# Performance work log

Measured on AMD Instinct MI355X. Metric: run time of the kernel, lower is better.

Reference implementation:

```python
import jax, jax.numpy as jnp
import numpy as np

B, K, D, V = 4096, 128, 512, 128000


def setup_inputs() -> dict:
    key = jax.random.key(0)
    k1, k2, k3 = jax.random.split(key, 3)
    inp = jax.random.normal(k1, (B, D), dtype=jnp.float32)
    indices = jax.random.randint(k2, (B, K), 0, V, dtype=jnp.int64)
    # xavier_uniform: bound = sqrt(6/(fan_in+fan_out)) for weight [V, D]
    bound = float(np.sqrt(6.0 / (V + D)))
    weight = jax.random.uniform(k3, (V, D), dtype=jnp.float32, minval=-bound, maxval=bound)
    bias = jnp.zeros((V,), dtype=jnp.float32)
    return {"inp": inp, "indices": indices, "sparse": 1, "weight": weight, "bias": bias}


def reference(inp, indices, sparse, weight, bias):
    if sparse:
        # gather per-sample weight rows [B, K, D] and bias [B, K], then batched dot
        w = weight[indices]          # [B, K, D]
        b = bias[indices]            # [B, K]
        out = jnp.einsum('bkd,bd->bk', w, inp) + b
        return out
    else:
        return inp @ weight.T + bias
```

## Files before the change

### kernel.cpp

```cpp
#include <hip/hip_runtime.h>
#include <stdint.h>


constexpr int Kc = 128;
constexpr int Dc = 512;
constexpr int Vc = 128000;

typedef float f4 __attribute__((ext_vector_type(4)));

__global__ __launch_bounds__(256) void SparseProjection_kernel(
    const float* __restrict__ inp,
    const int*   __restrict__ indices,
    const float* __restrict__ weight,
    const float* __restrict__ bias,
    float*       __restrict__ out)
{
    const int b    = blockIdx.x;
    const int tid  = threadIdx.x;
    const int lane = tid & 63;
    const int wave = tid >> 6;

    const float4* inp_row = (const float4*)(inp + (size_t)b * Dc);
    const float4 a0 = inp_row[lane];
    const float4 a1 = inp_row[64 + lane];

    const int* idx_base  = indices + (size_t)b * Kc;
    float*     out_base  = out     + (size_t)b * Kc;

    #pragma unroll 4
    for (int i = 0; i < 32; ++i) {
        const int k   = wave * 32 + i;
        const int idx = idx_base[k];
        const float4* wrow = (const float4*)(weight + (size_t)idx * Dc);

        const float4 w0 = wrow[lane];
        const float4 w1 = wrow[64 + lane];

        float s = a0.x * w0.x + a0.y * w0.y + a0.z * w0.z + a0.w * w0.w
                + a1.x * w1.x + a1.y * w1.y + a1.z * w1.z + a1.w * w1.w;

        #pragma unroll
        for (int off = 32; off > 0; off >>= 1)
            s += __shfl_xor(s, off, 64);

        if (lane == 0)
            out_base[k] = s + bias[idx];
    }
}


__global__ __launch_bounds__(256) void hist_kernel(
    const int* __restrict__ idx, unsigned int* __restrict__ counts, int n)
{
    int i      = blockIdx.x * blockDim.x + threadIdx.x;
    int stride = gridDim.x * blockDim.x;
    for (; i < n; i += stride)
        atomicAdd(&counts[idx[i]], 1u);
}

__global__ __launch_bounds__(256) void scan1_kernel(
    const unsigned int* __restrict__ counts, unsigned int* __restrict__ partials)
{
    __shared__ unsigned int sm[256];
    const int c = blockIdx.x;
    const int t = threadIdx.x;
    unsigned int a = counts[c * 512 + 2 * t] + counts[c * 512 + 2 * t + 1];
    sm[t] = a;
    __syncthreads();
    for (int off = 128; off > 0; off >>= 1) {
        if (t < off) sm[t] += sm[t + off];
        __syncthreads();
    }
    if (t == 0) partials[c] = sm[0];
}

__global__ __launch_bounds__(256) void scan2_kernel(
    unsigned int* __restrict__ partials, int nch)
{
    __shared__ unsigned int sm[256];
    const int t = threadIdx.x;
    unsigned int v = (t < nch) ? partials[t] : 0u;
    sm[t] = v;
    __syncthreads();
    for (int off = 1; off < 256; off <<= 1) {
        unsigned int add = (t >= off) ? sm[t - off] : 0u;
        __syncthreads();
        sm[t] += add;
        __syncthreads();
    }
    if (t < nch) partials[t] = sm[t] - v;
}

__global__ __launch_bounds__(256) void scan3_kernel(
    unsigned int* __restrict__ counts,
    const unsigned int* __restrict__ partials,
    unsigned int* __restrict__ starts,
    int n_total)
{
    __shared__ unsigned int sm[256];
    const int c    = blockIdx.x;
    const int t    = threadIdx.x;
    const int base = c * 512;
    unsigned int c0 = counts[base + 2 * t];
    unsigned int c1 = counts[base + 2 * t + 1];
    unsigned int pair = c0 + c1;
    sm[t] = pair;
    __syncthreads();
    for (int off = 1; off < 256; off <<= 1) {
        unsigned int add = (t >= off) ? sm[t - off] : 0u;
        __syncthreads();
        sm[t] += add;
        __syncthreads();
    }
    unsigned int excl = sm[t] - pair + partials[c];
    unsigned int s0 = excl;
    unsigned int s1 = excl + c0;
    starts[base + 2 * t]     = s0;
    starts[base + 2 * t + 1] = s1;
    counts[base + 2 * t]     = s0;
    counts[base + 2 * t + 1] = s1;
    if (c == 0 && t == 0) starts[Vc] = (unsigned int)n_total;
}

__global__ __launch_bounds__(256) void scatter_kernel(
    const int* __restrict__ idx, unsigned int* __restrict__ cursor,
    unsigned int* __restrict__ sorted, int n)
{
    int i      = blockIdx.x * blockDim.x + threadIdx.x;
    int stride = gridDim.x * blockDim.x;
    for (; i < n; i += stride) {
        int v = idx[i];
        unsigned int pos = atomicAdd(&cursor[v], 1u);
        sorted[pos] = (unsigned int)i;
    }
}

__device__ __forceinline__ float dot8(f4 a0, f4 a1, f4 w0, f4 w1) {
    return a0.x * w0.x + a0.y * w0.y + a0.z * w0.z + a0.w * w0.w
         + a1.x * w1.x + a1.y * w1.y + a1.z * w1.z + a1.w * w1.w;
}

__global__ __launch_bounds__(256) void compute_sorted_kernel(
    const float* __restrict__ inp,
    const float* __restrict__ weight,
    const float* __restrict__ bias,
    const unsigned int* __restrict__ starts,
    const unsigned int* __restrict__ sorted,
    float* __restrict__ out)
{
    const int lane = threadIdx.x & 63;
    const int wave = threadIdx.x >> 6;
    const int v    = blockIdx.x * 4 + wave;

    const unsigned int s = starts[v];
    const unsigned int e = starts[v + 1];
    if (s == e) return;

    const f4* wrow = (const f4*)(weight + (size_t)v * Dc);
    const f4 w0 = __builtin_nontemporal_load(wrow + lane);
    const f4 w1 = __builtin_nontemporal_load(wrow + 64 + lane);
    const float bv = bias[v];

    unsigned int j = s;
    for (; j + 2 <= e; j += 2) {
        const unsigned int bk0 = sorted[j];
        const unsigned int bk1 = sorted[j + 1];
        const f4* ar0 = (const f4*)(inp + (size_t)(bk0 >> 7) * Dc);
        const f4* ar1 = (const f4*)(inp + (size_t)(bk1 >> 7) * Dc);
        const f4 a00 = ar0[lane];
        const f4 a01 = ar0[64 + lane];
        const f4 a10 = ar1[lane];
        const f4 a11 = ar1[64 + lane];

        float s0 = dot8(a00, a01, w0, w1);
        float s1 = dot8(a10, a11, w0, w1);

        #pragma unroll
        for (int off = 32; off > 0; off >>= 1) {
            s0 += __shfl_xor(s0, off, 64);
            s1 += __shfl_xor(s1, off, 64);
        }

        if (lane == 0) {
            out[bk0] = s0 + bv;
            out[bk1] = s1 + bv;
        }
    }
    if (j < e) {
        const unsigned int bk = sorted[j];
        const f4* arow = (const f4*)(inp + (size_t)(bk >> 7) * Dc);
        const f4 a0 = arow[lane];
        const f4 a1 = arow[64 + lane];

        float sd = dot8(a0, a1, w0, w1);

        #pragma unroll
        for (int off = 32; off > 0; off >>= 1)
            sd += __shfl_xor(sd, off, 64);

        if (lane == 0)
            out[bk] = sd + bv;
    }
}

extern "C" void kernel_launch(void* const* d_in, const int* in_sizes, int n_in,
                              void* d_out, int out_size, void* d_ws, size_t ws_size,
                              hipStream_t stream) {
    const float* inp     = (const float*)d_in[0];
    const int*   indices = (const int*)  d_in[1];
    const float* weight  = (const float*)d_in[3];
    const float* bias    = (const float*)d_in[4];
    float*       out     = (float*)d_out;

    const int B = in_sizes[0] / Dc;
    const int n = B * Kc;

    const size_t need_u32 = (size_t)2 * Vc + 64 + (size_t)n + 256;
    if (ws_size < need_u32 * sizeof(unsigned int)) {
        SparseProjection_kernel<<<B, 256, 0, stream>>>(inp, indices, weight, bias, out);
        return;
    }

    unsigned int* ws       = (unsigned int*)d_ws;
    unsigned int* counts   = ws;
    unsigned int* starts   = ws + Vc;
    unsigned int* sorted   = ws + 2 * Vc + 64;
    unsigned int* partials = sorted + n;

    hipMemsetAsync(counts, 0, (size_t)Vc * sizeof(unsigned int), stream);

    hist_kernel<<<2048, 256, 0, stream>>>(indices, counts, n);
    scan1_kernel<<<Vc / 512, 256, 0, stream>>>(counts, partials);
    scan2_kernel<<<1, 256, 0, stream>>>(partials, Vc / 512);
    scan3_kernel<<<Vc / 512, 256, 0, stream>>>(counts, partials, starts, n);
    scatter_kernel<<<2048, 256, 0, stream>>>(indices, counts, sorted, n);

    compute_sorted_kernel<<<Vc / 4, 256, 0, stream>>>(inp, weight, bias, starts, sorted, out);
}
```

Before: 473.5 us.

## Vectorize index reads in histogram/scatter and split sorted compute into two passes

The histogram and scatter kernels now read indices as int4, issuing four atomics per thread, and launch fewer blocks. The compute kernel is launched twice over halves of the vocabulary so each pass touches a smaller weight range. Nontemporal weight loads are replaced with ordinary loads. A fallback is added for element counts not divisible by 1024. The split adds a launch and may not improve cache reuse of the input rows, which are shared across both halves.

Result: no change. 469.0 us (-1.0%).

```diff
diff --git a/kernel.cpp b/kernel.cpp
--- a/kernel.cpp
+++ b/kernel.cpp
@@ -5,6 +5,7 @@
 constexpr int Kc = 128;
 constexpr int Dc = 512;
 constexpr int Vc = 128000;
+constexpr int VSPLIT = 2;
 
 typedef float f4 __attribute__((ext_vector_type(4)));
 
@@ -50,12 +51,17 @@
 
 
 __global__ __launch_bounds__(256) void hist_kernel(
-    const int* __restrict__ idx, unsigned int* __restrict__ counts, int n)
+    const int4* __restrict__ idx4, unsigned int* __restrict__ counts, int n4)
 {
     int i      = blockIdx.x * blockDim.x + threadIdx.x;
     int stride = gridDim.x * blockDim.x;
-    for (; i < n; i += stride)
-        atomicAdd(&counts[idx[i]], 1u);
+    for (; i < n4; i += stride) {
+        int4 v = idx4[i];
+        atomicAdd(&counts[v.x], 1u);
+        atomicAdd(&counts[v.y], 1u);
+        atomicAdd(&counts[v.z], 1u);
+        atomicAdd(&counts[v.w], 1u);
+    }
 }
 
 __global__ __launch_bounds__(256) void scan1_kernel(
@@ -123,15 +129,19 @@
 }
 
 __global__ __launch_bounds__(256) void scatter_kernel(
-    const int* __restrict__ idx, unsigned int* __restrict__ cursor,
-    unsigned int* __restrict__ sorted, int n)
+    const int4* __restrict__ idx4, unsigned int* __restrict__ cursor,
+    unsigned int* __restrict__ sorted, int n4)
 {
     int i      = blockIdx.x * blockDim.x + threadIdx.x;
     int stride = gridDim.x * blockDim.x;
-    for (; i < n; i += stride) {
-        int v = idx[i];
-        unsigned int pos = atomicAdd(&cursor[v], 1u);
-        sorted[pos] = (unsigned int)i;
+    for (; i < n4; i += stride) {
+        int4 v = idx4[i];
+        unsigned int base = 4u * (unsigned int)i;
+        unsigned int p;
+        p = atomicAdd(&cursor[v.x], 1u); sorted[p] = base + 0;
+        p = atomicAdd(&cursor[v.y], 1u); sorted[p] = base + 1;
+        p = atomicAdd(&cursor[v.z], 1u); sorted[p] = base + 2;
+        p = atomicAdd(&cursor[v.w], 1u); sorted[p] = base + 3;
     }
 }
 
@@ -146,19 +156,20 @@
     const float* __restrict__ bias,
     const unsigned int* __restrict__ starts,
     const unsigned int* __restrict__ sorted,
-    float* __restrict__ out)
+    float* __restrict__ out,
+    int rowBase)
 {
     const int lane = threadIdx.x & 63;
     const int wave = threadIdx.x >> 6;
-    const int v    = blockIdx.x * 4 + wave;
+    const int v    = rowBase + blockIdx.x * 4 + wave;
 
     const unsigned int s = starts[v];
     const unsigned int e = starts[v + 1];
     if (s == e) return;
 
     const f4* wrow = (const f4*)(weight + (size_t)v * Dc);
-    const f4 w0 = __builtin_nontemporal_load(wrow + lane);
-    const f4 w1 = __builtin_nontemporal_load(wrow + 64 + lane);
+    const f4 w0 = wrow[lane];
+    const f4 w1 = wrow[64 + lane];
     const float bv = bias[v];
 
     unsigned int j = s;
@@ -216,7 +227,7 @@
     const int n = B * Kc;
 
     const size_t need_u32 = (size_t)2 * Vc + 64 + (size_t)n + 256;
-    if (ws_size < need_u32 * sizeof(unsigned int)) {
+    if ((n & 1023) != 0 || ws_size < need_u32 * sizeof(unsigned int)) {
         SparseProjection_kernel<<<B, 256, 0, stream>>>(inp, indices, weight, bias, out);
         return;
     }
@@ -227,13 +238,19 @@
     unsigned int* sorted   = ws + 2 * Vc + 64;
     unsigned int* partials = sorted + n;
 
+    const int n4 = n / 4;
+
     hipMemsetAsync(counts, 0, (size_t)Vc * sizeof(unsigned int), stream);
 
-    hist_kernel<<<2048, 256, 0, stream>>>(indices, counts, n);
+    hist_kernel<<<512, 256, 0, stream>>>((const int4*)indices, counts, n4);
     scan1_kernel<<<Vc / 512, 256, 0, stream>>>(counts, partials);
     scan2_kernel<<<1, 256, 0, stream>>>(partials, Vc / 512);
     scan3_kernel<<<Vc / 512, 256, 0, stream>>>(counts, partials, starts, n);
-    scatter_kernel<<<2048, 256, 0, stream>>>(indices, counts, sorted, n);
-
-    compute_sorted_kernel<<<Vc / 4, 256, 0, stream>>>(inp, weight, bias, starts, sorted, out);
-}
+    scatter_kernel<<<512, 256, 0, stream>>>((const int4*)indices, counts, sorted, n4);
+
+    const int rowsPerPass = Vc / VSPLIT;
+    for (int p = 0; p < VSPLIT; ++p) {
+        compute_sorted_kernel<<<rowsPerPass / 4, 256, 0, stream>>>(
+            inp, weight, bias, starts, sorted, out, p * rowsPerPass);
+    }
+}
```
